# Optimization experiments

Measured on AMD Instinct MI355X. Metric: run time of the kernel, lower is better.

Reference implementation:

```python
import jax, jax.numpy as jnp
import numpy as np

IN_FEATURES = 4096
OUT_FEATURES = 11008
GROUP_SIZE = 128
NUM_GROUPS = IN_FEATURES // GROUP_SIZE  # 32


def setup_inputs() -> dict:
    key = jax.random.key(0)
    k1, k2, k3, k4, k5 = jax.random.split(key, 5)
    x = jax.random.normal(k1, (4, 2048, IN_FEATURES), dtype=jnp.float16)
    # unpacked uint4 weight codes in [0, 15]
    qweight = jax.random.randint(k2, (OUT_FEATURES, IN_FEATURES), 0, 16, dtype=jnp.int32)
    scales = jax.random.uniform(k3, (NUM_GROUPS, OUT_FEATURES), dtype=jnp.float16)
    scaled_zeros = jax.random.normal(k4, (NUM_GROUPS, OUT_FEATURES), dtype=jnp.float16)
    bias = jax.random.normal(k5, (OUT_FEATURES,), dtype=jnp.float16)
    return {"x": x, "qweight": qweight, "scales": scales,
            "scaled_zeros": scaled_zeros, "bias": bias}


def reference(x, qweight, scales, scaled_zeros, bias):
    # Dequantize: w[o, g*gs + j] = q[o, g*gs + j] * scales[g, o] + scaled_zeros[g, o]
    oc, ic = qweight.shape
    ng = scales.shape[0]
    gs = ic // ng
    q = qweight.astype(scales.dtype).reshape(oc, ng, gs)          # [oc, ng, gs]
    w = q * scales.T[:, :, None] + scaled_zeros.T[:, :, None]     # [oc, ng, gs]
    w = w.reshape(oc, ic)                                         # [oc, ic]
    # out = x @ w^T + bias  (Linear semantics)
    out = jnp.einsum('bsi,oi->bso', x, w) + bias
    return out
```

## Files before the change

### kernel.cpp

```cpp
#include <hip/hip_runtime.h>
#include <hip/hip_bf16.h>

#define IC 4096
#define OC 11008
#define MTOT 8192

#define BM 256
#define BN 256
#define BK 64
#define NT (IC / BK)
#define LDSBUF 65536
#define BOFF 32768

typedef __attribute__((ext_vector_type(8))) short short8;
typedef __attribute__((ext_vector_type(4))) float floatx4;

__device__ __forceinline__ void async_copy16(const void* g, void* l) {
  __builtin_amdgcn_global_load_lds(
      (const __attribute__((address_space(1))) void*)g,
      (__attribute__((address_space(3))) void*)l, 16, 0, 0);
}

#define CFENCE() asm volatile("" ::: "memory")
#define BARRIER() do { CFENCE(); __builtin_amdgcn_s_barrier(); CFENCE(); } while (0)

__global__ __launch_bounds__(256) void cvt_x_kernel(
    const float* __restrict__ X, __hip_bfloat16* __restrict__ Xb) {
  size_t base = ((size_t)blockIdx.x * 256 + threadIdx.x) * 8;
  float4 a0 = *(const float4*)(X + base);
  float4 a1 = *(const float4*)(X + base + 4);
  union { __hip_bfloat16 h[8]; short8 v; } u;
  u.h[0] = __float2bfloat16(a0.x); u.h[1] = __float2bfloat16(a0.y);
  u.h[2] = __float2bfloat16(a0.z); u.h[3] = __float2bfloat16(a0.w);
  u.h[4] = __float2bfloat16(a1.x); u.h[5] = __float2bfloat16(a1.y);
  u.h[6] = __float2bfloat16(a1.z); u.h[7] = __float2bfloat16(a1.w);
  *(short8*)(Xb + base) = u.v;
}

__global__ __launch_bounds__(256) void dequant_kernel(
    const int* __restrict__ Q, const float* __restrict__ scales,
    const float* __restrict__ zeros, __hip_bfloat16* __restrict__ W) {
  size_t base = ((size_t)blockIdx.x * 256 + threadIdx.x) * 8;
  int o = (int)(base >> 12);
  int g = ((int)(base & 4095)) >> 7;
  float s = scales[(size_t)g * OC + o];
  float z = zeros[(size_t)g * OC + o];
  int4 q0 = *(const int4*)(Q + base);
  int4 q1 = *(const int4*)(Q + base + 4);
  union { __hip_bfloat16 h[8]; short8 v; } u;
  u.h[0] = __float2bfloat16(fmaf((float)q0.x, s, z));
  u.h[1] = __float2bfloat16(fmaf((float)q0.y, s, z));
  u.h[2] = __float2bfloat16(fmaf((float)q0.z, s, z));
  u.h[3] = __float2bfloat16(fmaf((float)q0.w, s, z));
  u.h[4] = __float2bfloat16(fmaf((float)q1.x, s, z));
  u.h[5] = __float2bfloat16(fmaf((float)q1.y, s, z));
  u.h[6] = __float2bfloat16(fmaf((float)q1.z, s, z));
  u.h[7] = __float2bfloat16(fmaf((float)q1.w, s, z));
  *(short8*)(W + base) = u.v;
}

__global__ __launch_bounds__(512, 2) void gemm_8phase(
    const __hip_bfloat16* __restrict__ A,
    const __hip_bfloat16* __restrict__ B,
    const float* __restrict__ bias,
    float* __restrict__ C) {
  __shared__ char lds[2 * LDSBUF];

  const int NBN = OC / BN;
  const int NBLK = (MTOT / BM) * NBN;
  int bid = blockIdx.x;
  int swz = (bid & 7) * (NBLK >> 3) + (bid >> 3);
  int bm = swz / NBN, bn = swz % NBN;
  const int m0 = bm * BM, n0 = bn * BN;

  const int tid  = threadIdx.x;
  const int lane = tid & 63;
  const int wid  = tid >> 6;
  const int wr = wid >> 2, wc = wid & 3;

  const int srl   = tid >> 3;
  const int scph  = (tid & 7) << 4;
  const int sclog = scph ^ ((srl & 7) << 4);
  const char* gA = (const char*)A + ((size_t)(m0 + srl) * IC) * 2 + sclog;
  const char* gB = (const char*)B + ((size_t)(n0 + srl) * IC) * 2 + sclog;
  const size_t UROW = (size_t)64 * IC * 2;
  const int sdst = tid * 16;

  const int l15  = lane & 15;
  const int hi16 = ((lane >> 4) & 3) << 4;
  const int swzl = (lane & 7) << 4;
  const int ck0  = hi16 ^ swzl;
  const int aRowB = (wr * 128 + l15) * 128;
  const int bRowB = (wc * 64  + l15) * 128;

  floatx4 acc[8][4];
#pragma unroll
  for (int i = 0; i < 8; ++i)
#pragma unroll
    for (int j = 0; j < 4; ++j)
      acc[i][j] = (floatx4){0.f, 0.f, 0.f, 0.f};

#pragma unroll
  for (int u = 0; u < 4; ++u)
    async_copy16(gA + u * UROW, lds + u * 8192 + sdst);
#pragma unroll
  for (int u = 0; u < 4; ++u)
    async_copy16(gB + u * UROW, lds + BOFF + u * 8192 + sdst);
#pragma unroll
  for (int u = 0; u < 4; ++u)
    async_copy16(gB + u * UROW + 128, lds + LDSBUF + BOFF + u * 8192 + sdst);
  async_copy16(gA + 0 * UROW + 128, lds + LDSBUF + 0 * 8192 + sdst);
  async_copy16(gA + 2 * UROW + 128, lds + LDSBUF + 2 * 8192 + sdst);
  asm volatile("s_waitcnt vmcnt(6)" ::: "memory");
  BARRIER();

  for (int t = 0; t < NT; ++t) {
    const int par = t & 1;
    char* curA = lds + par * LDSBUF;
    char* curB = curA + BOFF;
    char* nxtA = lds + (par ^ 1) * LDSBUF;
    const char* gAt1 = gA + (size_t)(t + 1) * 128;
    const char* gAt2 = gA + (size_t)(t + 2) * 128;
    const char* gBt2 = gB + (size_t)(t + 2) * 128;
    const bool s1 = (t + 1 < NT), s2 = (t + 2 < NT);

    const char* pa = curA + aRowB;
    const char* pb = curB + bRowB;
    short8 bfr[4][2];

#define MFMA16(P, AF0, AF1, AF2, AF3)                                        \
    BARRIER();                                                               \
    asm volatile("s_waitcnt lgkmcnt(0)" ::: "memory");                       \
    __builtin_amdgcn_s_setprio(1);                                           \
    _Pragma("unroll")                                                        \
    for (int fn = 0; fn < 4; ++fn) {                                         \
      acc[2*(P)][fn]   = __builtin_amdgcn_mfma_f32_16x16x32_bf16(            \
          AF0, bfr[fn][0], acc[2*(P)][fn], 0, 0, 0);                         \
      acc[2*(P)][fn]   = __builtin_amdgcn_mfma_f32_16x16x32_bf16(            \
          AF1, bfr[fn][1], acc[2*(P)][fn], 0, 0, 0);                         \
      acc[2*(P)+1][fn] = __builtin_amdgcn_mfma_f32_16x16x32_bf16(            \
          AF2, bfr[fn][0], acc[2*(P)+1][fn], 0, 0, 0);                       \
      acc[2*(P)+1][fn] = __builtin_amdgcn_mfma_f32_16x16x32_bf16(            \
          AF3, bfr[fn][1], acc[2*(P)+1][fn], 0, 0, 0);                       \
    }                                                                        \
    __builtin_amdgcn_s_setprio(0);

    {
      short8 a00 = *(const short8*)(pa + 0 * 2048 + ck0);
      short8 a01 = *(const short8*)(pa + 0 * 2048 + (ck0 ^ 64));
      short8 a10 = *(const short8*)(pa + 1 * 2048 + ck0);
      short8 a11 = *(const short8*)(pa + 1 * 2048 + (ck0 ^ 64));
#pragma unroll
      for (int fn = 0; fn < 4; ++fn) {
        bfr[fn][0] = *(const short8*)(pb + fn * 2048 + ck0);
        bfr[fn][1] = *(const short8*)(pb + fn * 2048 + (ck0 ^ 64));
      }
      if (s1) {
        async_copy16(gAt1 + 1 * UROW, nxtA + 1 * 8192 + sdst);
        async_copy16(gAt1 + 3 * UROW, nxtA + 3 * 8192 + sdst);
      }
      MFMA16(0, a00, a01, a10, a11);
      BARRIER();
    }
    {
      short8 a00 = *(const short8*)(pa + 2 * 2048 + ck0);
      short8 a01 = *(const short8*)(pa + 2 * 2048 + (ck0 ^ 64));
      short8 a10 = *(const short8*)(pa + 3 * 2048 + ck0);
      short8 a11 = *(const short8*)(pa + 3 * 2048 + (ck0 ^ 64));
      if (s2) {
        async_copy16(gBt2 + 0 * UROW, curB + 0 * 8192 + sdst);
        async_copy16(gBt2 + 1 * UROW, curB + 1 * 8192 + sdst);
      }
      MFMA16(1, a00, a01, a10, a11);
      BARRIER();
    }
    {
      short8 a00 = *(const short8*)(pa + 4 * 2048 + ck0);
      short8 a01 = *(const short8*)(pa + 4 * 2048 + (ck0 ^ 64));
      short8 a10 = *(const short8*)(pa + 5 * 2048 + ck0);
      short8 a11 = *(const short8*)(pa + 5 * 2048 + (ck0 ^ 64));
      if (s2) {
        async_copy16(gBt2 + 2 * UROW, curB + 2 * 8192 + sdst);
        async_copy16(gBt2 + 3 * UROW, curB + 3 * 8192 + sdst);
      }
      MFMA16(2, a00, a01, a10, a11);
      BARRIER();
    }
    {
      short8 a00 = *(const short8*)(pa + 6 * 2048 + ck0);
      short8 a01 = *(const short8*)(pa + 6 * 2048 + (ck0 ^ 64));
      short8 a10 = *(const short8*)(pa + 7 * 2048 + ck0);
      short8 a11 = *(const short8*)(pa + 7 * 2048 + (ck0 ^ 64));
      if (s2) {
        async_copy16(gAt2 + 0 * UROW, curA + 0 * 8192 + sdst);
        async_copy16(gAt2 + 2 * UROW, curA + 2 * 8192 + sdst);
      }
      MFMA16(3, a00, a01, a10, a11);
      if (s2)      { asm volatile("s_waitcnt vmcnt(6)" ::: "memory"); }
      else if (s1) { asm volatile("s_waitcnt vmcnt(0)" ::: "memory"); }
      BARRIER();
    }
#undef MFMA16
  }

#pragma unroll
  for (int fn = 0; fn < 4; ++fn) {
    int n = n0 + wc * 64 + fn * 16 + l15;
    float bv = bias[n];
#pragma unroll
    for (int fm = 0; fm < 8; ++fm) {
      int mrow = m0 + wr * 128 + fm * 16 + ((lane >> 4) << 2);
#pragma unroll
      for (int j = 0; j < 4; ++j)
        C[(size_t)(mrow + j) * OC + n] = acc[fm][fn][j] + bv;
    }
  }
}

__global__ __launch_bounds__(256) void w4_gemm_fused_f32(
    const float* __restrict__ A, const int* __restrict__ Q,
    const float* __restrict__ scales, const float* __restrict__ zeros,
    const float* __restrict__ bias, float* __restrict__ C) {
  __shared__ __hip_bfloat16 As[128 * 32];
  __shared__ __hip_bfloat16 Bs[128 * 32];
  const int NBN = OC / 128;
  const int NBLK = (MTOT / 128) * NBN;
  int bid = blockIdx.x;
  int swz = (bid & 7) * (NBLK >> 3) + (bid >> 3);
  int bm = swz / NBN, bn = swz % NBN;
  const int m0 = bm * 128, n0 = bn * 128;
  const int tid = threadIdx.x;
  const int wid = tid >> 6, lane = tid & 63;
  const int wr = wid >> 1, wc = wid & 1;
  const int row = tid >> 1;
  const int kh  = (tid & 1) * 16;
  const float* arow = A + (size_t)(m0 + row) * IC + kh;
  const int*   qrow = Q + (size_t)(n0 + row) * IC + kh;
  const int    nrow = n0 + row;
  const int a_row = wr * 64 + (lane & 15);
  const int b_row = wc * 64 + (lane & 15);
  const int frag_kb = (lane >> 4) * 16;
  floatx4 acc[4][4];
#pragma unroll
  for (int i = 0; i < 4; ++i)
#pragma unroll
    for (int j = 0; j < 4; ++j)
      acc[i][j] = (floatx4){0.f, 0.f, 0.f, 0.f};
  for (int k0 = 0; k0 < IC; k0 += 32) {
    float4 a0 = *(const float4*)(arow + k0);
    float4 a1 = *(const float4*)(arow + k0 + 4);
    float4 a2 = *(const float4*)(arow + k0 + 8);
    float4 a3 = *(const float4*)(arow + k0 + 12);
    int4 q0 = *(const int4*)(qrow + k0);
    int4 q1 = *(const int4*)(qrow + k0 + 4);
    int4 q2 = *(const int4*)(qrow + k0 + 8);
    int4 q3 = *(const int4*)(qrow + k0 + 12);
    int g = k0 >> 7;
    float s = scales[(size_t)g * OC + nrow];
    float z = zeros[(size_t)g * OC + nrow];
    union { __hip_bfloat16 h[16]; short8 v[2]; } ua, ub;
    ua.h[0]=__float2bfloat16(a0.x); ua.h[1]=__float2bfloat16(a0.y);
    ua.h[2]=__float2bfloat16(a0.z); ua.h[3]=__float2bfloat16(a0.w);
    ua.h[4]=__float2bfloat16(a1.x); ua.h[5]=__float2bfloat16(a1.y);
    ua.h[6]=__float2bfloat16(a1.z); ua.h[7]=__float2bfloat16(a1.w);
    ua.h[8]=__float2bfloat16(a2.x); ua.h[9]=__float2bfloat16(a2.y);
    ua.h[10]=__float2bfloat16(a2.z); ua.h[11]=__float2bfloat16(a2.w);
    ua.h[12]=__float2bfloat16(a3.x); ua.h[13]=__float2bfloat16(a3.y);
    ua.h[14]=__float2bfloat16(a3.z); ua.h[15]=__float2bfloat16(a3.w);
    ub.h[0]=__float2bfloat16(fmaf((float)q0.x,s,z));
    ub.h[1]=__float2bfloat16(fmaf((float)q0.y,s,z));
    ub.h[2]=__float2bfloat16(fmaf((float)q0.z,s,z));
    ub.h[3]=__float2bfloat16(fmaf((float)q0.w,s,z));
    ub.h[4]=__float2bfloat16(fmaf((float)q1.x,s,z));
    ub.h[5]=__float2bfloat16(fmaf((float)q1.y,s,z));
    ub.h[6]=__float2bfloat16(fmaf((float)q1.z,s,z));
    ub.h[7]=__float2bfloat16(fmaf((float)q1.w,s,z));
    ub.h[8]=__float2bfloat16(fmaf((float)q2.x,s,z));
    ub.h[9]=__float2bfloat16(fmaf((float)q2.y,s,z));
    ub.h[10]=__float2bfloat16(fmaf((float)q2.z,s,z));
    ub.h[11]=__float2bfloat16(fmaf((float)q2.w,s,z));
    ub.h[12]=__float2bfloat16(fmaf((float)q3.x,s,z));
    ub.h[13]=__float2bfloat16(fmaf((float)q3.y,s,z));
    ub.h[14]=__float2bfloat16(fmaf((float)q3.z,s,z));
    ub.h[15]=__float2bfloat16(fmaf((float)q3.w,s,z));
    *(short8*)(&As[row * 32 + kh])     = ua.v[0];
    *(short8*)(&As[row * 32 + kh + 8]) = ua.v[1];
    *(short8*)(&Bs[row * 32 + kh])     = ub.v[0];
    *(short8*)(&Bs[row * 32 + kh + 8]) = ub.v[1];
    __syncthreads();
    short8 af[4], bf[4];
#pragma unroll
    for (int fm = 0; fm < 4; ++fm)
      af[fm] = *(const short8*)((const char*)As + (a_row + fm*16)*64 + frag_kb);
#pragma unroll
    for (int fn = 0; fn < 4; ++fn)
      bf[fn] = *(const short8*)((const char*)Bs + (b_row + fn*16)*64 + frag_kb);
#pragma unroll
    for (int fm = 0; fm < 4; ++fm)
#pragma unroll
      for (int fn = 0; fn < 4; ++fn)
        acc[fm][fn] = __builtin_amdgcn_mfma_f32_16x16x32_bf16(
            af[fm], bf[fn], acc[fm][fn], 0, 0, 0);
    __syncthreads();
  }
#pragma unroll
  for (int fn = 0; fn < 4; ++fn) {
    int n = n0 + wc * 64 + fn * 16 + (lane & 15);
    float bv = bias[n];
#pragma unroll
    for (int fm = 0; fm < 4; ++fm) {
      int mrow = m0 + wr * 64 + fm * 16 + (lane >> 4) * 4;
#pragma unroll
      for (int j = 0; j < 4; ++j)
        C[(size_t)(mrow + j) * OC + n] = acc[fm][fn][j] + bv;
    }
  }
}

extern "C" void kernel_launch(void* const* d_in, const int* in_sizes, int n_in,
                              void* d_out, int out_size, void* d_ws, size_t ws_size,
                              hipStream_t stream) {
  const float* x      = (const float*)d_in[0];
  const int*   qw     = (const int*)d_in[1];
  const float* scales = (const float*)d_in[2];
  const float* szeros = (const float*)d_in[3];
  const float* bias   = (const float*)d_in[4];
  float* out = (float*)d_out;

  const size_t wbytes = (size_t)OC * IC * 2;
  const size_t xbytes = (size_t)MTOT * IC * 2;

  if (ws_size >= wbytes + xbytes) {
    __hip_bfloat16* W  = (__hip_bfloat16*)d_ws;
    __hip_bfloat16* Xb = (__hip_bfloat16*)((char*)d_ws + wbytes);
    cvt_x_kernel<<<16384, 256, 0, stream>>>(x, Xb);
    dequant_kernel<<<22016, 256, 0, stream>>>(qw, scales, szeros, W);
    gemm_8phase<<<1376, 512, 0, stream>>>(Xb, W, bias, out);
  } else {
    w4_gemm_fused_f32<<<5504, 256, 0, stream>>>(x, qw, scales, szeros, bias, out);
  }
}
```

Baseline: 755.6 us.

## Switch bf16 GEMM to 32x32x16 MFMA with B-fragment register prefetch

Replaces the 16x16x32 MFMA tiling with 32x32x16 MFMA instructions, giving each wave a 4x2 grid of 32x32 accumulators. The larger instruction needs fewer A/B fragment loads from LDS per FLOP. B fragments for the next K-tile are now read from LDS into registers during the second half of the current tile, so the B reads overlap with compute. The wait counts are rearranged to fit this. In exchange, register pressure rises from holding double-buffered B fragments, and the new LDS access pattern and waitcnt ordering could introduce bank conflicts or races.

```diff
diff --git a/kernel.cpp b/kernel.cpp
--- a/kernel.cpp
+++ b/kernel.cpp
@@ -14,6 +14,7 @@
 
 typedef __attribute__((ext_vector_type(8))) short short8;
 typedef __attribute__((ext_vector_type(4))) float floatx4;
+typedef __attribute__((ext_vector_type(16))) float floatx16;
 
 __device__ __forceinline__ void async_copy16(const void* g, void* l) {
   __builtin_amdgcn_global_load_lds(
@@ -86,19 +87,20 @@
   const size_t UROW = (size_t)64 * IC * 2;
   const int sdst = tid * 16;
 
-  const int l15  = lane & 15;
-  const int hi16 = ((lane >> 4) & 3) << 4;
-  const int swzl = (lane & 7) << 4;
-  const int ck0  = hi16 ^ swzl;
-  const int aRowB = (wr * 128 + l15) * 128;
-  const int bRowB = (wc * 64  + l15) * 128;
-
-  floatx4 acc[8][4];
-#pragma unroll
-  for (int i = 0; i < 8; ++i)
-#pragma unroll
-    for (int j = 0; j < 4; ++j)
-      acc[i][j] = (floatx4){0.f, 0.f, 0.f, 0.f};
+  const int l31 = lane & 31;
+  const int hi  = lane >> 5;
+  const int ck0 = (hi << 4) ^ ((lane & 7) << 4);
+  const int aBase = (wr * 128 + l31) * 128;
+  const int bBase = (wc * 64 + l31) * 128;
+
+  floatx16 acc[4][2];
+#pragma unroll
+  for (int i = 0; i < 4; ++i)
+#pragma unroll
+    for (int j = 0; j < 2; ++j)
+      acc[i][j] = (floatx16)(0.f);
+
+  short8 bcur[2][4], bnxt[2][4];
 
 #pragma unroll
   for (int u = 0; u < 4; ++u)
@@ -113,106 +115,136 @@
   async_copy16(gA + 2 * UROW + 128, lds + LDSBUF + 2 * 8192 + sdst);
   asm volatile("s_waitcnt vmcnt(6)" ::: "memory");
   BARRIER();
+  {
+    const char* pb0 = lds + BOFF + bBase;
+#pragma unroll
+    for (int cb = 0; cb < 2; ++cb)
+#pragma unroll
+      for (int s = 0; s < 4; ++s)
+        bnxt[cb][s] = *(const short8*)(pb0 + cb * 4096 + (ck0 ^ (s << 5)));
+  }
 
   for (int t = 0; t < NT; ++t) {
     const int par = t & 1;
     char* curA = lds + par * LDSBUF;
     char* curB = curA + BOFF;
     char* nxtA = lds + (par ^ 1) * LDSBUF;
+    char* nxtB = nxtA + BOFF;
     const char* gAt1 = gA + (size_t)(t + 1) * 128;
     const char* gAt2 = gA + (size_t)(t + 2) * 128;
     const char* gBt2 = gB + (size_t)(t + 2) * 128;
     const bool s1 = (t + 1 < NT), s2 = (t + 2 < NT);
 
-    const char* pa = curA + aRowB;
-    const char* pb = curB + bRowB;
-    short8 bfr[4][2];
-
-#define MFMA16(P, AF0, AF1, AF2, AF3)                                        \
+    const char* pa  = curA + aBase;
+    const char* pbn = nxtB + bBase;
+
+#pragma unroll
+    for (int cb = 0; cb < 2; ++cb)
+#pragma unroll
+      for (int s = 0; s < 4; ++s)
+        bcur[cb][s] = bnxt[cb][s];
+
+#define MFMA8(RB, SP, A00, A01, A10, A11)                                    \
     BARRIER();                                                               \
     asm volatile("s_waitcnt lgkmcnt(0)" ::: "memory");                       \
     __builtin_amdgcn_s_setprio(1);                                           \
-    _Pragma("unroll")                                                        \
-    for (int fn = 0; fn < 4; ++fn) {                                         \
-      acc[2*(P)][fn]   = __builtin_amdgcn_mfma_f32_16x16x32_bf16(            \
-          AF0, bfr[fn][0], acc[2*(P)][fn], 0, 0, 0);                         \
-      acc[2*(P)][fn]   = __builtin_amdgcn_mfma_f32_16x16x32_bf16(            \
-          AF1, bfr[fn][1], acc[2*(P)][fn], 0, 0, 0);                         \
-      acc[2*(P)+1][fn] = __builtin_amdgcn_mfma_f32_16x16x32_bf16(            \
-          AF2, bfr[fn][0], acc[2*(P)+1][fn], 0, 0, 0);                       \
-      acc[2*(P)+1][fn] = __builtin_amdgcn_mfma_f32_16x16x32_bf16(            \
-          AF3, bfr[fn][1], acc[2*(P)+1][fn], 0, 0, 0);                       \
-    }                                                                        \
+    acc[RB][0]     = __builtin_amdgcn_mfma_f32_32x32x16_bf16(                \
+        A00, bcur[0][SP], acc[RB][0], 0, 0, 0);                              \
+    acc[RB][1]     = __builtin_amdgcn_mfma_f32_32x32x16_bf16(                \
+        A00, bcur[1][SP], acc[RB][1], 0, 0, 0);                              \
+    acc[RB + 1][0] = __builtin_amdgcn_mfma_f32_32x32x16_bf16(                \
+        A10, bcur[0][SP], acc[RB + 1][0], 0, 0, 0);                          \
+    acc[RB + 1][1] = __builtin_amdgcn_mfma_f32_32x32x16_bf16(                \
+        A10, bcur[1][SP], acc[RB + 1][1], 0, 0, 0);                          \
+    acc[RB][0]     = __builtin_amdgcn_mfma_f32_32x32x16_bf16(                \
+        A01, bcur[0][SP + 1], acc[RB][0], 0, 0, 0);                          \
+    acc[RB][1]     = __builtin_amdgcn_mfma_f32_32x32x16_bf16(                \
+        A01, bcur[1][SP + 1], acc[RB][1], 0, 0, 0);                          \
+    acc[RB + 1][0] = __builtin_amdgcn_mfma_f32_32x32x16_bf16(                \
+        A11, bcur[0][SP + 1], acc[RB + 1][0], 0, 0, 0);                      \
+    acc[RB + 1][1] = __builtin_amdgcn_mfma_f32_32x32x16_bf16(                \
+        A11, bcur[1][SP + 1], acc[RB + 1][1], 0, 0, 0);                      \
     __builtin_amdgcn_s_setprio(0);
 
     {
-      short8 a00 = *(const short8*)(pa + 0 * 2048 + ck0);
-      short8 a01 = *(const short8*)(pa + 0 * 2048 + (ck0 ^ 64));
-      short8 a10 = *(const short8*)(pa + 1 * 2048 + ck0);
-      short8 a11 = *(const short8*)(pa + 1 * 2048 + (ck0 ^ 64));
-#pragma unroll
-      for (int fn = 0; fn < 4; ++fn) {
-        bfr[fn][0] = *(const short8*)(pb + fn * 2048 + ck0);
-        bfr[fn][1] = *(const short8*)(pb + fn * 2048 + (ck0 ^ 64));
-      }
+      short8 a00 = *(const short8*)(pa + 0 * 4096 + ck0);
+      short8 a01 = *(const short8*)(pa + 0 * 4096 + (ck0 ^ 32));
+      short8 a10 = *(const short8*)(pa + 1 * 4096 + ck0);
+      short8 a11 = *(const short8*)(pa + 1 * 4096 + (ck0 ^ 32));
       if (s1) {
         async_copy16(gAt1 + 1 * UROW, nxtA + 1 * 8192 + sdst);
         async_copy16(gAt1 + 3 * UROW, nxtA + 3 * 8192 + sdst);
       }
-      MFMA16(0, a00, a01, a10, a11);
+      MFMA8(0, 0, a00, a01, a10, a11);
       BARRIER();
     }
     {
-      short8 a00 = *(const short8*)(pa + 2 * 2048 + ck0);
-      short8 a01 = *(const short8*)(pa + 2 * 2048 + (ck0 ^ 64));
-      short8 a10 = *(const short8*)(pa + 3 * 2048 + ck0);
-      short8 a11 = *(const short8*)(pa + 3 * 2048 + (ck0 ^ 64));
+      short8 a00 = *(const short8*)(pa + 0 * 4096 + (ck0 ^ 64));
+      short8 a01 = *(const short8*)(pa + 0 * 4096 + (ck0 ^ 96));
+      short8 a10 = *(const short8*)(pa + 1 * 4096 + (ck0 ^ 64));
+      short8 a11 = *(const short8*)(pa + 1 * 4096 + (ck0 ^ 96));
       if (s2) {
         async_copy16(gBt2 + 0 * UROW, curB + 0 * 8192 + sdst);
         async_copy16(gBt2 + 1 * UROW, curB + 1 * 8192 + sdst);
       }
-      MFMA16(1, a00, a01, a10, a11);
+      MFMA8(0, 2, a00, a01, a10, a11);
       BARRIER();
     }
     {
-      short8 a00 = *(const short8*)(pa + 4 * 2048 + ck0);
-      short8 a01 = *(const short8*)(pa + 4 * 2048 + (ck0 ^ 64));
-      short8 a10 = *(const short8*)(pa + 5 * 2048 + ck0);
-      short8 a11 = *(const short8*)(pa + 5 * 2048 + (ck0 ^ 64));
+      short8 a00 = *(const short8*)(pa + 2 * 4096 + ck0);
+      short8 a01 = *(const short8*)(pa + 2 * 4096 + (ck0 ^ 32));
+      short8 a10 = *(const short8*)(pa + 3 * 4096 + ck0);
+      short8 a11 = *(const short8*)(pa + 3 * 4096 + (ck0 ^ 32));
+      if (s2)      { asm volatile("s_waitcnt vmcnt(6)" ::: "memory"); }
+      else if (s1) { asm volatile("s_waitcnt vmcnt(4)" ::: "memory"); }
       if (s2) {
         async_copy16(gBt2 + 2 * UROW, curB + 2 * 8192 + sdst);
         async_copy16(gBt2 + 3 * UROW, curB + 3 * 8192 + sdst);
       }
-      MFMA16(2, a00, a01, a10, a11);
+      MFMA8(2, 0, a00, a01, a10, a11);
+      if (s1) {
+        bnxt[0][0] = *(const short8*)(pbn + 0 * 4096 + (ck0 ^ 0));
+        bnxt[0][1] = *(const short8*)(pbn + 0 * 4096 + (ck0 ^ 32));
+        bnxt[0][2] = *(const short8*)(pbn + 0 * 4096 + (ck0 ^ 64));
+        bnxt[0][3] = *(const short8*)(pbn + 0 * 4096 + (ck0 ^ 96));
+      }
       BARRIER();
     }
     {
-      short8 a00 = *(const short8*)(pa + 6 * 2048 + ck0);
-      short8 a01 = *(const short8*)(pa + 6 * 2048 + (ck0 ^ 64));
-      short8 a10 = *(const short8*)(pa + 7 * 2048 + ck0);
-      short8 a11 = *(const short8*)(pa + 7 * 2048 + (ck0 ^ 64));
+      short8 a00 = *(const short8*)(pa + 2 * 4096 + (ck0 ^ 64));
+      short8 a01 = *(const short8*)(pa + 2 * 4096 + (ck0 ^ 96));
+      short8 a10 = *(const short8*)(pa + 3 * 4096 + (ck0 ^ 64));
+      short8 a11 = *(const short8*)(pa + 3 * 4096 + (ck0 ^ 96));
       if (s2) {
         async_copy16(gAt2 + 0 * UROW, curA + 0 * 8192 + sdst);
         async_copy16(gAt2 + 2 * UROW, curA + 2 * 8192 + sdst);
       }
-      MFMA16(3, a00, a01, a10, a11);
+      MFMA8(2, 2, a00, a01, a10, a11);
+      if (s1) {
+        bnxt[1][0] = *(const short8*)(pbn + 1 * 4096 + (ck0 ^ 0));
+        bnxt[1][1] = *(const short8*)(pbn + 1 * 4096 + (ck0 ^ 32));
+        bnxt[1][2] = *(const short8*)(pbn + 1 * 4096 + (ck0 ^ 64));
+        bnxt[1][3] = *(const short8*)(pbn + 1 * 4096 + (ck0 ^ 96));
+      }
       if (s2)      { asm volatile("s_waitcnt vmcnt(6)" ::: "memory"); }
       else if (s1) { asm volatile("s_waitcnt vmcnt(0)" ::: "memory"); }
       BARRIER();
     }
-#undef MFMA16
-  }
-
-#pragma unroll
-  for (int fn = 0; fn < 4; ++fn) {
-    int n = n0 + wc * 64 + fn * 16 + l15;
+#undef MFMA8
+  }
+
+#pragma unroll
+  for (int cb = 0; cb < 2; ++cb) {
+    int n = n0 + wc * 64 + cb * 32 + l31;
     float bv = bias[n];
 #pragma unroll
-    for (int fm = 0; fm < 8; ++fm) {
-      int mrow = m0 + wr * 128 + fm * 16 + ((lane >> 4) << 2);
-#pragma unroll
-      for (int j = 0; j < 4; ++j)
-        C[(size_t)(mrow + j) * OC + n] = acc[fm][fn][j] + bv;
+    for (int rb = 0; rb < 4; ++rb) {
+      int mbase = m0 + wr * 128 + rb * 32 + 4 * hi;
+#pragma unroll
+      for (int reg = 0; reg < 16; ++reg) {
+        int m = mbase + (reg & 3) + 8 * (reg >> 2);
+        C[(size_t)m * OC + n] = acc[rb][cb][reg] + bv;
+      }
     }
   }
 }
```

New measurement: 812.0 us. 7.5% more time.

## Split GEMM into 256x256 main kernel and 128x128 tail kernel for last columns

Applied to the files above, without the earlier changes.

The output columns are split in two. The first 10240 columns go to the existing 8-phase 256x256 GEMM, now launched with fewer blocks. The last 768 columns go to a new, simpler 128x128-tile MFMA kernel that is single-buffered with BK=32. The aim is to change how blocks fill the CUs across waves, but the tail kernel runs serially before the main one on the same stream and is a less efficient kernel, which adds its own time.

```diff
diff --git a/kernel.cpp b/kernel.cpp
--- a/kernel.cpp
+++ b/kernel.cpp
@@ -11,6 +11,12 @@
 #define NT (IC / BK)
 #define LDSBUF 65536
 #define BOFF 32768
+
+#define NBN_A 40
+#define NBLK_A 1280
+#define NBASE_B 10240
+#define NBN_B 6
+#define NBLK_B 384
 
 typedef __attribute__((ext_vector_type(8))) short short8;
 typedef __attribute__((ext_vector_type(4))) float floatx4;
@@ -66,11 +72,9 @@
     float* __restrict__ C) {
   __shared__ char lds[2 * LDSBUF];
 
-  const int NBN = OC / BN;
-  const int NBLK = (MTOT / BM) * NBN;
   int bid = blockIdx.x;
-  int swz = (bid & 7) * (NBLK >> 3) + (bid >> 3);
-  int bm = swz / NBN, bn = swz % NBN;
+  int swz = (bid & 7) * (NBLK_A >> 3) + (bid >> 3);
+  int bm = swz / NBN_A, bn = swz % NBN_A;
   const int m0 = bm * BM, n0 = bn * BN;
 
   const int tid  = threadIdx.x;
@@ -81,10 +85,11 @@
   const int srl   = tid >> 3;
   const int scph  = (tid & 7) << 4;
   const int sclog = scph ^ ((srl & 7) << 4);
+  const size_t UROW = (size_t)64 * IC * 2;
+  const int sdst = tid * 16;
+
   const char* gA = (const char*)A + ((size_t)(m0 + srl) * IC) * 2 + sclog;
   const char* gB = (const char*)B + ((size_t)(n0 + srl) * IC) * 2 + sclog;
-  const size_t UROW = (size_t)64 * IC * 2;
-  const int sdst = tid * 16;
 
   const int l15  = lane & 15;
   const int hi16 = ((lane >> 4) & 3) << 4;
@@ -210,6 +215,82 @@
 #pragma unroll
     for (int fm = 0; fm < 8; ++fm) {
       int mrow = m0 + wr * 128 + fm * 16 + ((lane >> 4) << 2);
+#pragma unroll
+      for (int j = 0; j < 4; ++j)
+        C[(size_t)(mrow + j) * OC + n] = acc[fm][fn][j] + bv;
+    }
+  }
+}
+
+__global__ __launch_bounds__(256) void gemm_bt_tail(
+    const __hip_bfloat16* __restrict__ A,
+    const __hip_bfloat16* __restrict__ B,
+    const float* __restrict__ bias,
+    float* __restrict__ C) {
+  __shared__ __hip_bfloat16 As[128 * 32];
+  __shared__ __hip_bfloat16 Bs[128 * 32];
+
+  int bid = blockIdx.x;
+  int swz = (bid & 7) * (NBLK_B >> 3) + (bid >> 3);
+  int bm = swz / NBN_B, bn = swz % NBN_B;
+  const int m0 = bm * 128, n0 = NBASE_B + bn * 128;
+
+  const int tid = threadIdx.x;
+  const int wid = tid >> 6, lane = tid & 63;
+  const int wr = wid >> 1, wc = wid & 1;
+
+  const int srow = lane >> 2;
+  const int scol = (lane & 3) * 8;
+
+  const int a_row = wr * 64 + (lane & 15);
+  const int b_row = wc * 64 + (lane & 15);
+  const int frag_kb = (lane >> 4) * 16;
+
+  floatx4 acc[4][4];
+#pragma unroll
+  for (int i = 0; i < 4; ++i)
+#pragma unroll
+    for (int j = 0; j < 4; ++j)
+      acc[i][j] = (floatx4){0.f, 0.f, 0.f, 0.f};
+
+  for (int k0 = 0; k0 < IC; k0 += 32) {
+#pragma unroll
+    for (int i = 0; i < 2; ++i) {
+      int s = wid * 2 + i;
+      const __hip_bfloat16* ga =
+          A + (size_t)(m0 + s * 16 + srow) * IC + k0 + scol;
+      async_copy16(ga, (char*)As + s * 1024);
+      const __hip_bfloat16* gb =
+          B + (size_t)(n0 + s * 16 + srow) * IC + k0 + scol;
+      async_copy16(gb, (char*)Bs + s * 1024);
+    }
+    __syncthreads();
+
+    short8 af[4], bf[4];
+#pragma unroll
+    for (int fm = 0; fm < 4; ++fm)
+      af[fm] = *(const short8*)((const char*)As + (a_row + fm * 16) * 64 + frag_kb);
+#pragma unroll
+    for (int fn = 0; fn < 4; ++fn)
+      bf[fn] = *(const short8*)((const char*)Bs + (b_row + fn * 16) * 64 + frag_kb);
+
+#pragma unroll
+    for (int fm = 0; fm < 4; ++fm)
+#pragma unroll
+      for (int fn = 0; fn < 4; ++fn)
+        acc[fm][fn] = __builtin_amdgcn_mfma_f32_16x16x32_bf16(
+            af[fm], bf[fn], acc[fm][fn], 0, 0, 0);
+
+    __syncthreads();
+  }
+
+#pragma unroll
+  for (int fn = 0; fn < 4; ++fn) {
+    int n = n0 + wc * 64 + fn * 16 + (lane & 15);
+    float bv = bias[n];
+#pragma unroll
+    for (int fm = 0; fm < 4; ++fm) {
+      int mrow = m0 + wr * 64 + fm * 16 + (lane >> 4) * 4;
 #pragma unroll
       for (int j = 0; j < 4; ++j)
         C[(size_t)(mrow + j) * OC + n] = acc[fm][fn][j] + bv;
@@ -335,7 +416,8 @@
     __hip_bfloat16* Xb = (__hip_bfloat16*)((char*)d_ws + wbytes);
     cvt_x_kernel<<<16384, 256, 0, stream>>>(x, Xb);
     dequant_kernel<<<22016, 256, 0, stream>>>(qw, scales, szeros, W);
-    gemm_8phase<<<1376, 512, 0, stream>>>(Xb, W, bias, out);
+    gemm_bt_tail<<<NBLK_B, 256, 0, stream>>>(Xb, W, bias, out);
+    gemm_8phase<<<NBLK_A, 512, 0, stream>>>(Xb, W, bias, out);
   } else {
     w4_gemm_fused_f32<<<5504, 256, 0, stream>>>(x, qw, scales, szeros, bias, out);
   }
```

Result: slower. 777.4 us (+2.9%).

## Split GEMM grid into 256-wide main tiles and 128-wide tail tiles

Applied to the files above, without the earlier changes.

The output's N dimension is split so the first 10240 columns use the existing 256x256 tiles. The remaining 768 columns are handled by a separate 256x128 tile path with half the B fragments and accumulators. The tail blocks get the lowest block IDs, and the main blocks use a recomputed swizzle over 40 N-tiles. The aim is to reshape the wave/occupancy distribution across CUs, at the cost of lower compute intensity in the narrower tail tiles and an extra code path.

```diff
diff --git a/kernel.cpp b/kernel.cpp
--- a/kernel.cpp
+++ b/kernel.cpp
@@ -11,6 +11,11 @@
 #define NT (IC / BK)
 #define LDSBUF 65536
 #define BOFF 32768
+
+#define NTAIL 192
+#define NBN_A 40
+#define NBLK_A 1280
+#define NBASE_T 10240
 
 typedef __attribute__((ext_vector_type(8))) short short8;
 typedef __attribute__((ext_vector_type(4))) float floatx4;
@@ -66,13 +71,6 @@
     float* __restrict__ C) {
   __shared__ char lds[2 * LDSBUF];
 
-  const int NBN = OC / BN;
-  const int NBLK = (MTOT / BM) * NBN;
-  int bid = blockIdx.x;
-  int swz = (bid & 7) * (NBLK >> 3) + (bid >> 3);
-  int bm = swz / NBN, bn = swz % NBN;
-  const int m0 = bm * BM, n0 = bn * BN;
-
   const int tid  = threadIdx.x;
   const int lane = tid & 63;
   const int wid  = tid >> 6;
@@ -81,8 +79,6 @@
   const int srl   = tid >> 3;
   const int scph  = (tid & 7) << 4;
   const int sclog = scph ^ ((srl & 7) << 4);
-  const char* gA = (const char*)A + ((size_t)(m0 + srl) * IC) * 2 + sclog;
-  const char* gB = (const char*)B + ((size_t)(n0 + srl) * IC) * 2 + sclog;
   const size_t UROW = (size_t)64 * IC * 2;
   const int sdst = tid * 16;
 
@@ -91,7 +87,146 @@
   const int swzl = (lane & 7) << 4;
   const int ck0  = hi16 ^ swzl;
   const int aRowB = (wr * 128 + l15) * 128;
-  const int bRowB = (wc * 64  + l15) * 128;
+
+  const int bid = blockIdx.x;
+
+  if (bid < NTAIL) {
+    const int bm = bid / 6, bn = bid % 6;
+    const int m0 = bm * BM, n0 = NBASE_T + bn * 128;
+
+    const char* gA = (const char*)A + ((size_t)(m0 + srl) * IC) * 2 + sclog;
+    const char* gB = (const char*)B + ((size_t)(n0 + srl) * IC) * 2 + sclog;
+    const int bRowB = (wc * 32 + l15) * 128;
+
+    floatx4 acc[8][2];
+#pragma unroll
+    for (int i = 0; i < 8; ++i)
+#pragma unroll
+      for (int j = 0; j < 2; ++j)
+        acc[i][j] = (floatx4){0.f, 0.f, 0.f, 0.f};
+
+#pragma unroll
+    for (int u = 0; u < 4; ++u)
+      async_copy16(gA + u * UROW, lds + u * 8192 + sdst);
+#pragma unroll
+    for (int u = 0; u < 2; ++u)
+      async_copy16(gB + u * UROW, lds + BOFF + u * 8192 + sdst);
+#pragma unroll
+    for (int u = 0; u < 2; ++u)
+      async_copy16(gB + u * UROW + 128, lds + LDSBUF + BOFF + u * 8192 + sdst);
+    async_copy16(gA + 0 * UROW + 128, lds + LDSBUF + 0 * 8192 + sdst);
+    async_copy16(gA + 2 * UROW + 128, lds + LDSBUF + 2 * 8192 + sdst);
+    asm volatile("s_waitcnt vmcnt(4)" ::: "memory");
+    BARRIER();
+
+    for (int t = 0; t < NT; ++t) {
+      const int par = t & 1;
+      char* curA = lds + par * LDSBUF;
+      char* curB = curA + BOFF;
+      char* nxtA = lds + (par ^ 1) * LDSBUF;
+      const char* gAt1 = gA + (size_t)(t + 1) * 128;
+      const char* gAt2 = gA + (size_t)(t + 2) * 128;
+      const char* gBt2 = gB + (size_t)(t + 2) * 128;
+      const bool s1 = (t + 1 < NT), s2 = (t + 2 < NT);
+
+      const char* pa = curA + aRowB;
+      const char* pb = curB + bRowB;
+      short8 bfr[2][2];
+
+#define MFMA8T(P, AF0, AF1, AF2, AF3)                                        \
+      BARRIER();                                                             \
+      asm volatile("s_waitcnt lgkmcnt(0)" ::: "memory");                     \
+      __builtin_amdgcn_s_setprio(1);                                         \
+      _Pragma("unroll")                                                      \
+      for (int fn = 0; fn < 2; ++fn) {                                       \
+        acc[2*(P)][fn]   = __builtin_amdgcn_mfma_f32_16x16x32_bf16(          \
+            AF0, bfr[fn][0], acc[2*(P)][fn], 0, 0, 0);                       \
+        acc[2*(P)][fn]   = __builtin_amdgcn_mfma_f32_16x16x32_bf16(          \
+            AF1, bfr[fn][1], acc[2*(P)][fn], 0, 0, 0);                       \
+        acc[2*(P)+1][fn] = __builtin_amdgcn_mfma_f32_16x16x32_bf16(          \
+            AF2, bfr[fn][0], acc[2*(P)+1][fn], 0, 0, 0);                     \
+        acc[2*(P)+1][fn] = __builtin_amdgcn_mfma_f32_16x16x32_bf16(          \
+            AF3, bfr[fn][1], acc[2*(P)+1][fn], 0, 0, 0);                     \
+      }                                                                      \
+      __builtin_amdgcn_s_setprio(0);
+
+      {
+        short8 a00 = *(const short8*)(pa + 0 * 2048 + ck0);
+        short8 a01 = *(const short8*)(pa + 0 * 2048 + (ck0 ^ 64));
+        short8 a10 = *(const short8*)(pa + 1 * 2048 + ck0);
+        short8 a11 = *(const short8*)(pa + 1 * 2048 + (ck0 ^ 64));
+#pragma unroll
+        for (int fn = 0; fn < 2; ++fn) {
+          bfr[fn][0] = *(const short8*)(pb + fn * 2048 + ck0);
+          bfr[fn][1] = *(const short8*)(pb + fn * 2048 + (ck0 ^ 64));
+        }
+        if (s1) {
+          async_copy16(gAt1 + 1 * UROW, nxtA + 1 * 8192 + sdst);
+          async_copy16(gAt1 + 3 * UROW, nxtA + 3 * 8192 + sdst);
+        }
+        MFMA8T(0, a00, a01, a10, a11);
+        BARRIER();
+      }
+      {
+        short8 a00 = *(const short8*)(pa + 2 * 2048 + ck0);
+        short8 a01 = *(const short8*)(pa + 2 * 2048 + (ck0 ^ 64));
+        short8 a10 = *(const short8*)(pa + 3 * 2048 + ck0);
+        short8 a11 = *(const short8*)(pa + 3 * 2048 + (ck0 ^ 64));
+        if (s2) {
+          async_copy16(gBt2 + 0 * UROW, curB + 0 * 8192 + sdst);
+          async_copy16(gBt2 + 1 * UROW, curB + 1 * 8192 + sdst);
+        }
+        MFMA8T(1, a00, a01, a10, a11);
+        BARRIER();
+      }
+      {
+        short8 a00 = *(const short8*)(pa + 4 * 2048 + ck0);
+        short8 a01 = *(const short8*)(pa + 4 * 2048 + (ck0 ^ 64));
+        short8 a10 = *(const short8*)(pa + 5 * 2048 + ck0);
+        short8 a11 = *(const short8*)(pa + 5 * 2048 + (ck0 ^ 64));
+        if (s2) {
+          async_copy16(gAt2 + 0 * UROW, curA + 0 * 8192 + sdst);
+          async_copy16(gAt2 + 2 * UROW, curA + 2 * 8192 + sdst);
+        }
+        MFMA8T(2, a00, a01, a10, a11);
+        BARRIER();
+      }
+      {
+        short8 a00 = *(const short8*)(pa + 6 * 2048 + ck0);
+        short8 a01 = *(const short8*)(pa + 6 * 2048 + (ck0 ^ 64));
+        short8 a10 = *(const short8*)(pa + 7 * 2048 + ck0);
+        short8 a11 = *(const short8*)(pa + 7 * 2048 + (ck0 ^ 64));
+        MFMA8T(3, a00, a01, a10, a11);
+        if (s2)      { asm volatile("s_waitcnt vmcnt(4)" ::: "memory"); }
+        else if (s1) { asm volatile("s_waitcnt vmcnt(0)" ::: "memory"); }
+        BARRIER();
+      }
+#undef MFMA8T
+    }
+
+#pragma unroll
+    for (int fn = 0; fn < 2; ++fn) {
+      int n = n0 + wc * 32 + fn * 16 + l15;
+      float bv = bias[n];
+#pragma unroll
+      for (int fm = 0; fm < 8; ++fm) {
+        int mrow = m0 + wr * 128 + fm * 16 + ((lane >> 4) << 2);
+#pragma unroll
+        for (int j = 0; j < 4; ++j)
+          C[(size_t)(mrow + j) * OC + n] = acc[fm][fn][j] + bv;
+      }
+    }
+    return;
+  }
+
+  int mb = bid - NTAIL;
+  int swz = (mb & 7) * (NBLK_A >> 3) + (mb >> 3);
+  int bm = swz / NBN_A, bn = swz % NBN_A;
+  const int m0 = bm * BM, n0 = bn * BN;
+
+  const char* gA = (const char*)A + ((size_t)(m0 + srl) * IC) * 2 + sclog;
+  const char* gB = (const char*)B + ((size_t)(n0 + srl) * IC) * 2 + sclog;
+  const int bRowB = (wc * 64 + l15) * 128;
 
   floatx4 acc[8][4];
 #pragma unroll
@@ -335,7 +470,7 @@
     __hip_bfloat16* Xb = (__hip_bfloat16*)((char*)d_ws + wbytes);
     cvt_x_kernel<<<16384, 256, 0, stream>>>(x, Xb);
     dequant_kernel<<<22016, 256, 0, stream>>>(qw, scales, szeros, W);
-    gemm_8phase<<<1376, 512, 0, stream>>>(Xb, W, bias, out);
+    gemm_8phase<<<NTAIL + NBLK_A, 512, 0, stream>>>(Xb, W, bias, out);
   } else {
     w4_gemm_fused_f32<<<5504, 256, 0, stream>>>(x, qw, scales, szeros, bias, out);
   }
```

New measurement: 769.0 us. About the same (+1.8%).
